# Optimization experiments

Hardware: AMD Instinct MI355X
Metric: run time of the kernel (lower is better)

Reference implementation:

```python
import jax, jax.numpy as jnp
import numpy as np

IN_FEATURES = 4096
OUT_FEATURES = 11008
BATCH = 16


def setup_inputs() -> dict:
    key = jax.random.key(0)
    k_x, k_w, k_s, k_b = jax.random.split(key, 4)
    x = jax.random.normal(k_x, (BATCH, IN_FEATURES), dtype=jnp.float32)
    # symmetric int8 weights stored as int32 for jax portability (values in [-127, 127])
    weight_int8 = jax.random.randint(k_w, (OUT_FEATURES, IN_FEATURES), -127, 128, dtype=jnp.int32)
    # per-output-channel scales, small positive values typical of int8 quantization
    weight_scale = jax.random.uniform(k_s, (OUT_FEATURES,), dtype=jnp.float32, minval=0.005, maxval=0.02)
    bias = jax.random.normal(k_b, (OUT_FEATURES,), dtype=jnp.float32)
    return {"x": x, "weight_int8": weight_int8, "weight_scale": weight_scale, "bias": bias}


def reference(x, weight_int8, weight_scale, bias):
    # Dequantize: w_dq[o, i] = int8[o, i] * scale[o]  -> fp32 [OUT, IN]
    w_dq = weight_int8.astype(x.dtype) * weight_scale[:, None]
    # F.linear: y = x @ w_dq.T + bias  -> [BATCH, OUT]
    return jnp.einsum("bi,oi->bo", x, w_dq) + bias
```

## Files before the change

kernel.cpp:

```cpp
#include <hip/hip_runtime.h>

#define IN_F   4096
#define OUT_F  11008
#define BATCH  16
#define TK     512
#define CO     16
#define BLOCK  256
#define SPLITK 4
#define KCHUNK (IN_F / SPLITK)

typedef int   i32x4 __attribute__((ext_vector_type(4)));

__global__ __launch_bounds__(BLOCK) void init_out_kernel(
    const float* __restrict__ bias, float* __restrict__ out)
{
    int idx = blockIdx.x * BLOCK + threadIdx.x;
    if (idx < BATCH * OUT_F) {
        int o = idx % OUT_F;
        out[idx] = bias[o];
    }
}

__global__ __launch_bounds__(BLOCK) void qlin_kernel(
    const float* __restrict__ x,
    const int*   __restrict__ w,
    const float* __restrict__ scale,
    float* __restrict__ out)
{
    __shared__ float xs[BATCH][TK];

    const int tid = threadIdx.x;
    const int tx  = tid & 63;
    const int ty  = tid >> 6;
    const int o0  = blockIdx.x * CO + ty * 4;
    const int kb  = blockIdx.y * KCHUNK;

    const i32x4* __restrict__ wbase = (const i32x4*)(w + (size_t)o0 * IN_F);

    float acc[64];
    #pragma unroll
    for (int i = 0; i < 64; ++i) acc[i] = 0.f;

    for (int k0 = kb; k0 < kb + KCHUNK; k0 += TK) {
        #pragma unroll
        for (int j = 0; j < (BATCH * TK / 4) / BLOCK; ++j) {
            int f  = tid + j * BLOCK;
            int b  = f >> 7;
            int kc = f & 127;
            const float* src = x + (size_t)b * IN_F + k0 + kc * 4;
            void* dst = (char*)&xs[0][0] + (size_t)f * 16;
            __builtin_amdgcn_global_load_lds(
                (const __attribute__((address_space(1))) void*)src,
                (__attribute__((address_space(3))) void*)dst,
                16, 0, 0);
        }
        __syncthreads();

        #pragma unroll
        for (int it = 0; it < TK / 256; ++it) {
            const int    kl  = it * 256 + tx * 4;
            const size_t kg4 = (size_t)((k0 >> 2) + it * 64 + tx);

            i32x4 w0 = __builtin_nontemporal_load(wbase + kg4);
            i32x4 w1 = __builtin_nontemporal_load(wbase + kg4 + 1 * (IN_F / 4));
            i32x4 w2 = __builtin_nontemporal_load(wbase + kg4 + 2 * (IN_F / 4));
            i32x4 w3 = __builtin_nontemporal_load(wbase + kg4 + 3 * (IN_F / 4));

            float wf[4][4];
            #pragma unroll
            for (int e = 0; e < 4; ++e) {
                wf[0][e] = (float)w0[e];
                wf[1][e] = (float)w1[e];
                wf[2][e] = (float)w2[e];
                wf[3][e] = (float)w3[e];
            }

            #pragma unroll
            for (int bc = 0; bc < 4; ++bc) {
                float4 xv[4];
                #pragma unroll
                for (int bb = 0; bb < 4; ++bb)
                    xv[bb] = *(const float4*)&xs[bc * 4 + bb][kl];

                #pragma unroll
                for (int r = 0; r < 4; ++r)
                    #pragma unroll
                    for (int bb = 0; bb < 4; ++bb) {
                        float a = acc[r * 16 + bc * 4 + bb];
                        a += wf[r][0] * xv[bb].x;
                        a += wf[r][1] * xv[bb].y;
                        a += wf[r][2] * xv[bb].z;
                        a += wf[r][3] * xv[bb].w;
                        acc[r * 16 + bc * 4 + bb] = a;
                    }
            }
        }
        __syncthreads();
    }

    #pragma unroll
    for (int wd = 32; wd >= 1; wd >>= 1) {
        const bool upper = (tx & wd) != 0;
        #pragma unroll
        for (int i = 0; i < wd; ++i) {
            float lo = acc[i]      + __shfl_xor(acc[i],      wd);
            float hi = acc[i + wd] + __shfl_xor(acc[i + wd], wd);
            acc[i] = upper ? hi : lo;
        }
    }

    const int o = o0 + (tx >> 4);
    const int b = tx & 15;
    atomicAdd(&out[(size_t)b * OUT_F + o], acc[0] * scale[o]);
}

extern "C" void kernel_launch(void* const* d_in, const int* in_sizes, int n_in,
                              void* d_out, int out_size, void* d_ws, size_t ws_size,
                              hipStream_t stream) {
    const float* x     = (const float*)d_in[0];
    const int*   w     = (const int*)d_in[1];
    const float* scale = (const float*)d_in[2];
    const float* bias  = (const float*)d_in[3];
    float* out = (float*)d_out;

    init_out_kernel<<<(BATCH * OUT_F + BLOCK - 1) / BLOCK, BLOCK, 0, stream>>>(bias, out);

    dim3 grid(OUT_F / CO, SPLITK);
    qlin_kernel<<<grid, dim3(BLOCK), 0, stream>>>(x, w, scale, out);
}
```

Measured before the change: 259.3 us.

## Double split-K and hoist all weight loads ahead of the x staging

Split-K goes from 4 to 8, so each block covers a 512-wide K chunk and the K loop reduces to a single pass. All eight weight vector loads are issued up front, before the global-to-LDS staging of x and the barrier, so their memory latency overlaps the x load and the wait. In exchange the grid doubles, which doubles the atomicAdd traffic on the output and the x reloads, and register pressure rises from holding the weights early.

```diff
diff --git a/kernel.cpp b/kernel.cpp
--- a/kernel.cpp
+++ b/kernel.cpp
@@ -3,13 +3,12 @@
 #define IN_F   4096
 #define OUT_F  11008
 #define BATCH  16
-#define TK     512
 #define CO     16
 #define BLOCK  256
-#define SPLITK 4
+#define SPLITK 8
 #define KCHUNK (IN_F / SPLITK)
 
-typedef int   i32x4 __attribute__((ext_vector_type(4)));
+typedef int i32x4 __attribute__((ext_vector_type(4)));
 
 __global__ __launch_bounds__(BLOCK) void init_out_kernel(
     const float* __restrict__ bias, float* __restrict__ out)
@@ -27,7 +26,7 @@
     const float* __restrict__ scale,
     float* __restrict__ out)
 {
-    __shared__ float xs[BATCH][TK];
+    __shared__ float xs[BATCH][KCHUNK];
 
     const int tid = threadIdx.x;
     const int tx  = tid & 63;
@@ -37,65 +36,64 @@
 
     const i32x4* __restrict__ wbase = (const i32x4*)(w + (size_t)o0 * IN_F);
 
+    i32x4 wv[2][4];
+    #pragma unroll
+    for (int it = 0; it < 2; ++it) {
+        const size_t kg4 = (size_t)((kb >> 2) + it * 64 + tx);
+        #pragma unroll
+        for (int r = 0; r < 4; ++r)
+            wv[it][r] = __builtin_nontemporal_load(wbase + kg4 + (size_t)r * (IN_F / 4));
+    }
+
+    #pragma unroll
+    for (int j = 0; j < (BATCH * KCHUNK / 4) / BLOCK; ++j) {
+        int f  = tid + j * BLOCK;
+        int b  = f >> 7;
+        int kc = f & 127;
+        const float* src = x + (size_t)b * IN_F + kb + kc * 4;
+        void* dst = (char*)&xs[0][0] + (size_t)f * 16;
+        __builtin_amdgcn_global_load_lds(
+            (const __attribute__((address_space(1))) void*)src,
+            (__attribute__((address_space(3))) void*)dst,
+            16, 0, 0);
+    }
+
+    __syncthreads();
+
     float acc[64];
     #pragma unroll
     for (int i = 0; i < 64; ++i) acc[i] = 0.f;
 
-    for (int k0 = kb; k0 < kb + KCHUNK; k0 += TK) {
+    #pragma unroll
+    for (int it = 0; it < 2; ++it) {
+        const int kl = it * 256 + tx * 4;
+
+        float wf[4][4];
         #pragma unroll
-        for (int j = 0; j < (BATCH * TK / 4) / BLOCK; ++j) {
-            int f  = tid + j * BLOCK;
-            int b  = f >> 7;
-            int kc = f & 127;
-            const float* src = x + (size_t)b * IN_F + k0 + kc * 4;
-            void* dst = (char*)&xs[0][0] + (size_t)f * 16;
-            __builtin_amdgcn_global_load_lds(
-                (const __attribute__((address_space(1))) void*)src,
-                (__attribute__((address_space(3))) void*)dst,
-                16, 0, 0);
-        }
-        __syncthreads();
+        for (int r = 0; r < 4; ++r)
+            #pragma unroll
+            for (int e = 0; e < 4; ++e)
+                wf[r][e] = (float)wv[it][r][e];
 
         #pragma unroll
-        for (int it = 0; it < TK / 256; ++it) {
-            const int    kl  = it * 256 + tx * 4;
-            const size_t kg4 = (size_t)((k0 >> 2) + it * 64 + tx);
-
-            i32x4 w0 = __builtin_nontemporal_load(wbase + kg4);
-            i32x4 w1 = __builtin_nontemporal_load(wbase + kg4 + 1 * (IN_F / 4));
-            i32x4 w2 = __builtin_nontemporal_load(wbase + kg4 + 2 * (IN_F / 4));
-            i32x4 w3 = __builtin_nontemporal_load(wbase + kg4 + 3 * (IN_F / 4));
-
-            float wf[4][4];
+        for (int bc = 0; bc < 4; ++bc) {
+            float4 xv[4];
             #pragma unroll
-            for (int e = 0; e < 4; ++e) {
-                wf[0][e] = (float)w0[e];
-                wf[1][e] = (float)w1[e];
-                wf[2][e] = (float)w2[e];
-                wf[3][e] = (float)w3[e];
-            }
+            for (int bb = 0; bb < 4; ++bb)
+                xv[bb] = *(const float4*)&xs[bc * 4 + bb][kl];
 
             #pragma unroll
-            for (int bc = 0; bc < 4; ++bc) {
-                float4 xv[4];
+            for (int r = 0; r < 4; ++r)
                 #pragma unroll
-                for (int bb = 0; bb < 4; ++bb)
-                    xv[bb] = *(const float4*)&xs[bc * 4 + bb][kl];
-
-                #pragma unroll
-                for (int r = 0; r < 4; ++r)
-                    #pragma unroll
-                    for (int bb = 0; bb < 4; ++bb) {
-                        float a = acc[r * 16 + bc * 4 + bb];
-                        a += wf[r][0] * xv[bb].x;
-                        a += wf[r][1] * xv[bb].y;
-                        a += wf[r][2] * xv[bb].z;
-                        a += wf[r][3] * xv[bb].w;
-                        acc[r * 16 + bc * 4 + bb] = a;
-                    }
-            }
+                for (int bb = 0; bb < 4; ++bb) {
+                    float a = acc[r * 16 + bc * 4 + bb];
+                    a += wf[r][0] * xv[bb].x;
+                    a += wf[r][1] * xv[bb].y;
+                    a += wf[r][2] * xv[bb].z;
+                    a += wf[r][3] * xv[bb].w;
+                    acc[r * 16 + bc * 4 + bb] = a;
+                }
         }
-        __syncthreads();
     }
 
     #pragma unroll
```

Result: slower. 266.7 us (+2.8%).
